# Kernel tuning notes

Hardware: AMD Instinct MI355X
Metric: run time of the kernel (lower is better)

Reference implementation:

```python
import jax, jax.numpy as jnp
import numpy as np

NUM_BINS = 24


def setup_inputs() -> dict:
    key = jax.random.key(0)
    k1, k2 = jax.random.split(key)
    x = jax.random.normal(k1, (64, 1, 512, 512), dtype=jnp.float32)
    y = jax.random.normal(k2, (64, 1, 512, 512), dtype=jnp.float32)
    return {"x": x, "y": y}


def reference(x, y):
    nb = NUM_BINS
    B = x.shape[0]
    # torch.no_grad() downsample -> stop_gradient
    xs = jax.lax.stop_gradient(x[:, :, ::2, ::2])
    ys = jax.lax.stop_gradient(y[:, :, ::2, ::2])
    # small additive noise (randn_like * 1e-4), fixed key for determinism
    nk1, nk2 = jax.random.split(jax.random.key(42))
    xs = xs + jax.random.normal(nk1, xs.shape, xs.dtype) * 0.0001
    ys = ys + jax.random.normal(nk2, ys.shape, ys.dtype) * 0.0001
    x_flat = xs.reshape(B, -1)
    y_flat = ys.reshape(B, -1)
    x_flat = jnp.clip((x_flat + 1.0) * 0.5, 0.001, 0.999)
    y_flat = jnp.clip((y_flat + 1.0) * 0.5, 0.001, 0.999)
    # bucketize against linspace(0,1,nb+1) minus 1 == floor(v*nb), clamped
    x_bin = jnp.clip(jnp.floor(x_flat * nb).astype(jnp.int32), 0, nb - 1)
    y_bin = jnp.clip(jnp.floor(y_flat * nb).astype(jnp.int32), 0, nb - 1)
    # joint histogram for all batches at once via one segment_sum
    batch_off = (jnp.arange(B, dtype=jnp.int32) * (nb * nb))[:, None]
    seg = (batch_off + x_bin * nb + y_bin).reshape(-1)
    ones = jnp.ones(seg.shape, dtype=jnp.float32)
    hist = jax.ops.segment_sum(ones, seg, num_segments=B * nb * nb)
    joint = hist.reshape(B, nb, nb)
    total = joint.sum(axis=(1, 2), keepdims=True) + 1e-10
    joint = joint / total  # [B, nb, nb]
    x_hist = joint.sum(axis=2)  # [B, nb]
    y_hist = joint.sum(axis=1)  # [B, nb]
    eps = 1e-05
    joint_e = joint + eps
    xh = x_hist + eps
    yh = y_hist + eps
    log_joint = jnp.log(joint_e)
    log_prod = jnp.log(xh[:, :, None] * yh[:, None, :])
    mi = jnp.sum(joint_e * (log_joint - log_prod), axis=(1, 2))  # [B]
    hx = -jnp.sum(xh * jnp.log(xh), axis=1)
    hy = -jnp.sum(yh * jnp.log(yh), axis=1)
    se = hx + hy
    nmi = jnp.where(se < 1e-10, 0.0, 2.0 * mi / se)
    nmi = jnp.clip(nmi, -1.0, 1.0)
    return -jnp.clip(jnp.mean(nmi), -1.0, 1.0)
```

## Files before the change

### kernel.cpp

```cpp
#include <hip/hip_runtime.h>
#include <stdint.h>
#include <stddef.h>


#define NB 24
#define NBINS 576
#define NBATCH 64
#define SPB 65536
#define HIST_BPB 16
#define HIST_THREADS 512
#define PER_BLOCK 4096
#define QCAP 1024
#define MARGIN 0.008f

__host__ __device__ __forceinline__ uint32_t rotl32_(uint32_t x, uint32_t r) {
  return (x << r) | (x >> (32u - r));
}

__host__ __device__ inline void threefry2x32_(uint32_t k0, uint32_t k1,
                                              uint32_t& x0, uint32_t& x1) {
  const uint32_t k2 = k0 ^ k1 ^ 0x1BD11BDAu;
  x0 += k0; x1 += k1;
#define TFR(r) { x0 += x1; x1 = rotl32_(x1, (r)); x1 ^= x0; }
  TFR(13u) TFR(15u) TFR(26u) TFR(6u)
  x0 += k1; x1 += k2 + 1u;
  TFR(17u) TFR(29u) TFR(16u) TFR(24u)
  x0 += k2; x1 += k0 + 2u;
  TFR(13u) TFR(15u) TFR(26u) TFR(6u)
  x0 += k0; x1 += k1 + 3u;
  TFR(17u) TFR(29u) TFR(16u) TFR(24u)
  x0 += k1; x1 += k2 + 4u;
  TFR(13u) TFR(15u) TFR(26u) TFR(6u)
  x0 += k2; x1 += k0 + 5u;
#undef TFR
}

__device__ __forceinline__ float erfinv32_(float x) {
  float w = -log1pf(-x * x);
  float p;
  if (w < 5.0f) {
    w -= 2.5f;
    p =  2.81022636e-08f;
    p = fmaf(p, w,  3.43273939e-07f);
    p = fmaf(p, w, -3.5233877e-06f);
    p = fmaf(p, w, -4.39150654e-06f);
    p = fmaf(p, w,  0.00021858087f);
    p = fmaf(p, w, -0.00125372503f);
    p = fmaf(p, w, -0.00417768164f);
    p = fmaf(p, w,  0.246640727f);
    p = fmaf(p, w,  1.50140941f);
  } else {
    w = sqrtf(w) - 3.0f;
    p = -0.000200214257f;
    p = fmaf(p, w,  0.000100950558f);
    p = fmaf(p, w,  0.00134934322f);
    p = fmaf(p, w, -0.00367342844f);
    p = fmaf(p, w,  0.00573950773f);
    p = fmaf(p, w, -0.0076224613f);
    p = fmaf(p, w,  0.00943887047f);
    p = fmaf(p, w,  1.00167406f);
    p = fmaf(p, w,  2.83297682f);
  }
  return p * x;
}

__device__ __forceinline__ float tf_normal_(uint32_t ka, uint32_t kb, uint32_t n) {
  uint32_t x0 = 0u, x1 = n;
  threefry2x32_(ka, kb, x0, x1);
  const uint32_t bits = x0 ^ x1;
  float f = __uint_as_float((bits >> 9) | 0x3F800000u) - 1.0f;
  const float lo = -0.99999994f;
  float u = f * 2.0f + lo;
  u = fmaxf(lo, u);
  return 1.41421356f * erfinv32_(u);
}

__global__ __launch_bounds__(HIST_THREADS) void nmi_hist_kernel(
    const float* __restrict__ x, const float* __restrict__ y,
    uint32_t* __restrict__ ghist,
    uint32_t nk1a, uint32_t nk1b, uint32_t nk2a, uint32_t nk2b) {
  __shared__ uint32_t h[NBINS];
  __shared__ uint16_t q[QCAP];
  __shared__ uint32_t qn;
  for (int t = threadIdx.x; t < NBINS; t += HIST_THREADS) h[t] = 0u;
  if (threadIdx.x == 0) qn = 0u;
  __syncthreads();

  const int b    = blockIdx.x / HIST_BPB;
  const int blk  = blockIdx.x % HIST_BPB;
  const int base = blk * PER_BLOCK;
  const float* __restrict__ xb = x + (size_t)b * 262144;
  const float* __restrict__ yb = y + (size_t)b * 262144;
  const uint32_t nbase = (uint32_t)b * (uint32_t)SPB;

  #pragma unroll
  for (int k = 0; k < PER_BLOCK / HIST_THREADS; ++k) {
    const int i = k * HIST_THREADS + (int)threadIdx.x;
    const int s = base + i;
    const int src = ((s >> 8) << 10) + ((s & 255) << 1);
    const float xv = xb[src];
    const float yv = yb[src];
    const float tx = fminf(fmaxf((xv + 1.0f) * 0.5f, 0.001f), 0.999f) * 24.0f;
    const float ty = fminf(fmaxf((yv + 1.0f) * 0.5f, 0.001f), 0.999f) * 24.0f;
    const float fx = floorf(tx), fy = floorf(ty);
    const float rx = tx - fx,   ry = ty - fy;
    const bool safe = (rx >= MARGIN) & (rx <= 1.0f - MARGIN) &
                      (ry >= MARGIN) & (ry <= 1.0f - MARGIN);
    if (safe) {
      atomicAdd(&h[(int)fx * NB + (int)fy], 1u);
    } else {
      const uint32_t qi = atomicAdd(&qn, 1u);
      if (qi < QCAP) {
        q[qi] = (uint16_t)i;
      } else {
        const uint32_t n = nbase + (uint32_t)s;
        const float xn = xv + tf_normal_(nk1a, nk1b, n) * 1e-4f;
        const float yn = yv + tf_normal_(nk2a, nk2b, n) * 1e-4f;
        const float vx = fminf(fmaxf((xn + 1.0f) * 0.5f, 0.001f), 0.999f);
        const float vy = fminf(fmaxf((yn + 1.0f) * 0.5f, 0.001f), 0.999f);
        int bx = (int)floorf(vx * 24.0f);
        int by = (int)floorf(vy * 24.0f);
        bx = bx < 0 ? 0 : (bx > 23 ? 23 : bx);
        by = by < 0 ? 0 : (by > 23 ? 23 : by);
        atomicAdd(&h[bx * NB + by], 1u);
      }
    }
  }
  __syncthreads();

  const uint32_t nq = qn < QCAP ? qn : (uint32_t)QCAP;
  for (uint32_t j = threadIdx.x; j < nq; j += HIST_THREADS) {
    const int i = (int)q[j];
    const int s = base + i;
    const int src = ((s >> 8) << 10) + ((s & 255) << 1);
    const uint32_t n = nbase + (uint32_t)s;
    const float xn = xb[src] + tf_normal_(nk1a, nk1b, n) * 1e-4f;
    const float yn = yb[src] + tf_normal_(nk2a, nk2b, n) * 1e-4f;
    const float vx = fminf(fmaxf((xn + 1.0f) * 0.5f, 0.001f), 0.999f);
    const float vy = fminf(fmaxf((yn + 1.0f) * 0.5f, 0.001f), 0.999f);
    int bx = (int)floorf(vx * 24.0f);
    int by = (int)floorf(vy * 24.0f);
    bx = bx < 0 ? 0 : (bx > 23 ? 23 : bx);
    by = by < 0 ? 0 : (by > 23 ? 23 : by);
    atomicAdd(&h[bx * NB + by], 1u);
  }
  __syncthreads();

  uint32_t* gh = ghist + b * NBINS;
  for (int t = threadIdx.x; t < NBINS; t += HIST_THREADS) {
    const uint32_t c = h[t];
    if (c) atomicAdd(&gh[t], c);
  }
}

__global__ __launch_bounds__(256) void nmi_reduce_kernel(
    const uint32_t* __restrict__ ghist, float* __restrict__ nmi_arr,
    uint32_t* __restrict__ ctr, float* __restrict__ out) {
  const int b = blockIdx.x;
  __shared__ float joint[NBINS];
  __shared__ float xh[NB];
  __shared__ float yh[NB];
  __shared__ float red_mi[4];
  __shared__ float red_h[4];
  __shared__ int islast;

  const uint32_t* gh = ghist + b * NBINS;
  for (int t = threadIdx.x; t < NBINS; t += 256)
    joint[t] = (float)gh[t] * (1.0f / 65536.0f);
  __syncthreads();

  if (threadIdx.x < NB) {
    const int i = threadIdx.x;
    float sx = 0.f, sy = 0.f;
    for (int j = 0; j < NB; ++j) {
      sx += joint[i * NB + j];
      sy += joint[j * NB + i];
    }
    xh[i] = sx; yh[i] = sy;
  }
  __syncthreads();

  float mi_part = 0.f;
  for (int t = threadIdx.x; t < NBINS; t += 256) {
    const int i = t / NB, j = t % NB;
    const float je = joint[t] + 1e-5f;
    const float pe = (xh[i] + 1e-5f) * (yh[j] + 1e-5f);
    mi_part += je * (logf(je) - logf(pe));
  }
  float h_part = 0.f;
  if (threadIdx.x < NB) {
    const float e = xh[threadIdx.x] + 1e-5f;
    h_part = -(e * logf(e));
  } else if (threadIdx.x >= 64 && threadIdx.x < 64 + NB) {
    const float e = yh[threadIdx.x - 64] + 1e-5f;
    h_part = -(e * logf(e));
  }

  for (int o = 32; o > 0; o >>= 1) {
    mi_part += __shfl_down(mi_part, o);
    h_part  += __shfl_down(h_part, o);
  }
  const int wid  = threadIdx.x >> 6;
  const int lane = threadIdx.x & 63;
  if (lane == 0) { red_mi[wid] = mi_part; red_h[wid] = h_part; }
  __syncthreads();

  if (threadIdx.x == 0) {
    const float mi = red_mi[0] + red_mi[1] + red_mi[2] + red_mi[3];
    const float se = red_h[0] + red_h[1] + red_h[2] + red_h[3];
    float nmi = (se < 1e-10f) ? 0.0f : (2.0f * mi / se);
    nmi = fminf(fmaxf(nmi, -1.0f), 1.0f);
    __hip_atomic_store(&nmi_arr[b], nmi, __ATOMIC_RELEASE,
                       __HIP_MEMORY_SCOPE_AGENT);
    const uint32_t t = __hip_atomic_fetch_add(ctr, 1u, __ATOMIC_ACQ_REL,
                                              __HIP_MEMORY_SCOPE_AGENT);
    islast = (t == (uint32_t)(NBATCH - 1));
  }
  __syncthreads();

  if (islast && threadIdx.x < 64) {
    float v = __hip_atomic_load(&nmi_arr[threadIdx.x], __ATOMIC_ACQUIRE,
                                __HIP_MEMORY_SCOPE_AGENT);
    for (int o = 32; o > 0; o >>= 1) v += __shfl_down(v, o);
    if (threadIdx.x == 0) {
      float m = v * (1.0f / 64.0f);
      m = fminf(fmaxf(m, -1.0f), 1.0f);
      out[0] = -m;
    }
  }
}

extern "C" void kernel_launch(void* const* d_in, const int* in_sizes, int n_in,
                              void* d_out, int out_size, void* d_ws, size_t ws_size,
                              hipStream_t stream) {
  const float* x = (const float*)d_in[0];
  const float* y = (const float*)d_in[1];
  float* out = (float*)d_out;

  uint32_t* ghist = (uint32_t*)d_ws;
  uint32_t* ctr   = (uint32_t*)((char*)d_ws + 147456);
  float*    nmi   = (float*)((char*)d_ws + 147520);

  uint32_t nk1a = 0u, nk1b = 0u; threefry2x32_(0u, 42u, nk1a, nk1b);
  uint32_t nk2a = 0u, nk2b = 1u; threefry2x32_(0u, 42u, nk2a, nk2b);

  hipMemsetAsync(d_ws, 0, 147520 + NBATCH * sizeof(float), stream);
  nmi_hist_kernel<<<NBATCH * HIST_BPB, HIST_THREADS, 0, stream>>>(
      x, y, ghist, nk1a, nk1b, nk2a, nk2b);
  nmi_reduce_kernel<<<NBATCH, 256, 0, stream>>>(ghist, nmi, ctr, out);
}
```

Measured before the change: 138.2 us.

## Fuse histogram and NMI reduction via per-batch last-block completion counters

Merges the histogram and reduce kernels into one launch. Each block writes its partial histogram to its own slot, and the last block per batch (found through an atomic counter) sums the 16 partials and computes the NMI. A global counter lets the final block produce the mean, and the memset shrinks to just the counters. Loads are widened to float4 so each thread handles two strided samples from one vector read, which fetches both even and odd columns and doubles the bytes read per useful sample. The change removes a launch and the global histogram atomics, at the cost of a serialized tail in the last blocks.

```diff
diff --git a/kernel.cpp b/kernel.cpp
--- a/kernel.cpp
+++ b/kernel.cpp
@@ -12,6 +12,11 @@
 #define PER_BLOCK 4096
 #define QCAP 1024
 #define MARGIN 0.008f
+
+#define PART_ELEMS (NBATCH * HIST_BPB * NBINS)
+#define CTR_OFF   ((size_t)PART_ELEMS * 4)
+#define GCTR_OFF  (CTR_OFF + 256)
+#define NMI_OFF   (CTR_OFF + 512)
 
 __host__ __device__ __forceinline__ uint32_t rotl32_(uint32_t x, uint32_t r) {
   return (x << r) | (x >> (32u - r));
@@ -75,15 +80,25 @@
   return 1.41421356f * erfinv32_(u);
 }
 
-__global__ __launch_bounds__(HIST_THREADS) void nmi_hist_kernel(
+__global__ __launch_bounds__(HIST_THREADS) void nmi_fused_kernel(
     const float* __restrict__ x, const float* __restrict__ y,
-    uint32_t* __restrict__ ghist,
+    uint32_t* __restrict__ part, uint32_t* __restrict__ ctr,
+    uint32_t* __restrict__ gctr, float* __restrict__ nmi_arr,
+    float* __restrict__ out,
     uint32_t nk1a, uint32_t nk1b, uint32_t nk2a, uint32_t nk2b) {
   __shared__ uint32_t h[NBINS];
   __shared__ uint16_t q[QCAP];
   __shared__ uint32_t qn;
-  for (int t = threadIdx.x; t < NBINS; t += HIST_THREADS) h[t] = 0u;
-  if (threadIdx.x == 0) qn = 0u;
+  __shared__ int islast, glast;
+  __shared__ float joint[NBINS];
+  __shared__ float xh[NB];
+  __shared__ float yh[NB];
+  __shared__ float red_mi[8];
+  __shared__ float red_h[8];
+
+  const int tid = threadIdx.x;
+  for (int t = tid; t < NBINS; t += HIST_THREADS) h[t] = 0u;
+  if (tid == 0) qn = 0u;
   __syncthreads();
 
   const int b    = blockIdx.x / HIST_BPB;
@@ -94,42 +109,50 @@
   const uint32_t nbase = (uint32_t)b * (uint32_t)SPB;
 
   #pragma unroll
-  for (int k = 0; k < PER_BLOCK / HIST_THREADS; ++k) {
-    const int i = k * HIST_THREADS + (int)threadIdx.x;
-    const int s = base + i;
-    const int src = ((s >> 8) << 10) + ((s & 255) << 1);
-    const float xv = xb[src];
-    const float yv = yb[src];
-    const float tx = fminf(fmaxf((xv + 1.0f) * 0.5f, 0.001f), 0.999f) * 24.0f;
-    const float ty = fminf(fmaxf((yv + 1.0f) * 0.5f, 0.001f), 0.999f) * 24.0f;
-    const float fx = floorf(tx), fy = floorf(ty);
-    const float rx = tx - fx,   ry = ty - fy;
-    const bool safe = (rx >= MARGIN) & (rx <= 1.0f - MARGIN) &
-                      (ry >= MARGIN) & (ry <= 1.0f - MARGIN);
-    if (safe) {
-      atomicAdd(&h[(int)fx * NB + (int)fy], 1u);
-    } else {
-      const uint32_t qi = atomicAdd(&qn, 1u);
-      if (qi < QCAP) {
-        q[qi] = (uint16_t)i;
+  for (int k = 0; k < PER_BLOCK / (2 * HIST_THREADS); ++k) {
+    const int p  = k * HIST_THREADS + tid;
+    const int s0 = base + 2 * p;
+    const int hh = s0 >> 8;
+    const int ww = s0 & 255;
+    const int src = (hh << 10) + (ww << 1);
+    const float4 xv4 = *reinterpret_cast<const float4*>(xb + src);
+    const float4 yv4 = *reinterpret_cast<const float4*>(yb + src);
+    #pragma unroll
+    for (int e = 0; e < 2; ++e) {
+      const float xv = e ? xv4.z : xv4.x;
+      const float yv = e ? yv4.z : yv4.x;
+      const int   i  = 2 * p + e;
+      const float tx = fminf(fmaxf((xv + 1.0f) * 0.5f, 0.001f), 0.999f) * 24.0f;
+      const float ty = fminf(fmaxf((yv + 1.0f) * 0.5f, 0.001f), 0.999f) * 24.0f;
+      const float fx = floorf(tx), fy = floorf(ty);
+      const float rx = tx - fx,   ry = ty - fy;
+      const bool safe = (rx >= MARGIN) & (rx <= 1.0f - MARGIN) &
+                        (ry >= MARGIN) & (ry <= 1.0f - MARGIN);
+      if (safe) {
+        atomicAdd(&h[(int)fx * NB + (int)fy], 1u);
       } else {
-        const uint32_t n = nbase + (uint32_t)s;
-        const float xn = xv + tf_normal_(nk1a, nk1b, n) * 1e-4f;
-        const float yn = yv + tf_normal_(nk2a, nk2b, n) * 1e-4f;
-        const float vx = fminf(fmaxf((xn + 1.0f) * 0.5f, 0.001f), 0.999f);
-        const float vy = fminf(fmaxf((yn + 1.0f) * 0.5f, 0.001f), 0.999f);
-        int bx = (int)floorf(vx * 24.0f);
-        int by = (int)floorf(vy * 24.0f);
-        bx = bx < 0 ? 0 : (bx > 23 ? 23 : bx);
-        by = by < 0 ? 0 : (by > 23 ? 23 : by);
-        atomicAdd(&h[bx * NB + by], 1u);
+        const uint32_t qi = atomicAdd(&qn, 1u);
+        if (qi < QCAP) {
+          q[qi] = (uint16_t)i;
+        } else {
+          const uint32_t n = nbase + (uint32_t)(base + i);
+          const float xn = xv + tf_normal_(nk1a, nk1b, n) * 1e-4f;
+          const float yn = yv + tf_normal_(nk2a, nk2b, n) * 1e-4f;
+          const float vx = fminf(fmaxf((xn + 1.0f) * 0.5f, 0.001f), 0.999f);
+          const float vy = fminf(fmaxf((yn + 1.0f) * 0.5f, 0.001f), 0.999f);
+          int bx = (int)floorf(vx * 24.0f);
+          int by = (int)floorf(vy * 24.0f);
+          bx = bx < 0 ? 0 : (bx > 23 ? 23 : bx);
+          by = by < 0 ? 0 : (by > 23 ? 23 : by);
+          atomicAdd(&h[bx * NB + by], 1u);
+        }
       }
     }
   }
   __syncthreads();
 
   const uint32_t nq = qn < QCAP ? qn : (uint32_t)QCAP;
-  for (uint32_t j = threadIdx.x; j < nq; j += HIST_THREADS) {
+  for (uint32_t j = tid; j < nq; j += HIST_THREADS) {
     const int i = (int)q[j];
     const int s = base + i;
     const int src = ((s >> 8) << 10) + ((s & 255) << 1);
@@ -146,53 +169,54 @@
   }
   __syncthreads();
 
-  uint32_t* gh = ghist + b * NBINS;
-  for (int t = threadIdx.x; t < NBINS; t += HIST_THREADS) {
-    const uint32_t c = h[t];
-    if (c) atomicAdd(&gh[t], c);
-  }
-}
-
-__global__ __launch_bounds__(256) void nmi_reduce_kernel(
-    const uint32_t* __restrict__ ghist, float* __restrict__ nmi_arr,
-    uint32_t* __restrict__ ctr, float* __restrict__ out) {
-  const int b = blockIdx.x;
-  __shared__ float joint[NBINS];
-  __shared__ float xh[NB];
-  __shared__ float yh[NB];
-  __shared__ float red_mi[4];
-  __shared__ float red_h[4];
-  __shared__ int islast;
-
-  const uint32_t* gh = ghist + b * NBINS;
-  for (int t = threadIdx.x; t < NBINS; t += 256)
-    joint[t] = (float)gh[t] * (1.0f / 65536.0f);
-  __syncthreads();
-
-  if (threadIdx.x < NB) {
-    const int i = threadIdx.x;
+  uint32_t* gp = part + (size_t)(b * HIST_BPB + blk) * NBINS;
+  for (int t = tid; t < NBINS; t += HIST_THREADS)
+    __hip_atomic_store(&gp[t], h[t], __ATOMIC_RELAXED,
+                       __HIP_MEMORY_SCOPE_AGENT);
+  __syncthreads();
+
+  if (tid == 0) {
+    const uint32_t t = __hip_atomic_fetch_add(&ctr[b], 1u, __ATOMIC_ACQ_REL,
+                                              __HIP_MEMORY_SCOPE_AGENT);
+    islast = (t == (uint32_t)(HIST_BPB - 1));
+  }
+  __syncthreads();
+  if (!islast) return;
+
+  const uint32_t* pb = part + (size_t)b * HIST_BPB * NBINS;
+  for (int t = tid; t < NBINS; t += HIST_THREADS) {
+    uint32_t c = 0;
+    #pragma unroll
+    for (int sb = 0; sb < HIST_BPB; ++sb)
+      c += __hip_atomic_load(&pb[sb * NBINS + t], __ATOMIC_RELAXED,
+                             __HIP_MEMORY_SCOPE_AGENT);
+    joint[t] = (float)c * (1.0f / 65536.0f);
+  }
+  __syncthreads();
+
+  if (tid < NB) {
     float sx = 0.f, sy = 0.f;
     for (int j = 0; j < NB; ++j) {
-      sx += joint[i * NB + j];
-      sy += joint[j * NB + i];
+      sx += joint[tid * NB + j];
+      sy += joint[j * NB + tid];
     }
-    xh[i] = sx; yh[i] = sy;
+    xh[tid] = sx; yh[tid] = sy;
   }
   __syncthreads();
 
   float mi_part = 0.f;
-  for (int t = threadIdx.x; t < NBINS; t += 256) {
+  for (int t = tid; t < NBINS; t += HIST_THREADS) {
     const int i = t / NB, j = t % NB;
     const float je = joint[t] + 1e-5f;
     const float pe = (xh[i] + 1e-5f) * (yh[j] + 1e-5f);
     mi_part += je * (logf(je) - logf(pe));
   }
   float h_part = 0.f;
-  if (threadIdx.x < NB) {
-    const float e = xh[threadIdx.x] + 1e-5f;
+  if (tid < NB) {
+    const float e = xh[tid] + 1e-5f;
     h_part = -(e * logf(e));
-  } else if (threadIdx.x >= 64 && threadIdx.x < 64 + NB) {
-    const float e = yh[threadIdx.x - 64] + 1e-5f;
+  } else if (tid >= 64 && tid < 64 + NB) {
+    const float e = yh[tid - 64] + 1e-5f;
     h_part = -(e * logf(e));
   }
 
@@ -200,29 +224,30 @@
     mi_part += __shfl_down(mi_part, o);
     h_part  += __shfl_down(h_part, o);
   }
-  const int wid  = threadIdx.x >> 6;
-  const int lane = threadIdx.x & 63;
+  const int wid  = tid >> 6;
+  const int lane = tid & 63;
   if (lane == 0) { red_mi[wid] = mi_part; red_h[wid] = h_part; }
   __syncthreads();
 
-  if (threadIdx.x == 0) {
-    const float mi = red_mi[0] + red_mi[1] + red_mi[2] + red_mi[3];
-    const float se = red_h[0] + red_h[1] + red_h[2] + red_h[3];
+  if (tid == 0) {
+    float mi = 0.f, se = 0.f;
+    #pragma unroll
+    for (int w = 0; w < HIST_THREADS / 64; ++w) { mi += red_mi[w]; se += red_h[w]; }
     float nmi = (se < 1e-10f) ? 0.0f : (2.0f * mi / se);
     nmi = fminf(fmaxf(nmi, -1.0f), 1.0f);
     __hip_atomic_store(&nmi_arr[b], nmi, __ATOMIC_RELEASE,
                        __HIP_MEMORY_SCOPE_AGENT);
-    const uint32_t t = __hip_atomic_fetch_add(ctr, 1u, __ATOMIC_ACQ_REL,
-                                              __HIP_MEMORY_SCOPE_AGENT);
-    islast = (t == (uint32_t)(NBATCH - 1));
-  }
-  __syncthreads();
-
-  if (islast && threadIdx.x < 64) {
-    float v = __hip_atomic_load(&nmi_arr[threadIdx.x], __ATOMIC_ACQUIRE,
+    const uint32_t t2 = __hip_atomic_fetch_add(gctr, 1u, __ATOMIC_ACQ_REL,
+                                               __HIP_MEMORY_SCOPE_AGENT);
+    glast = (t2 == (uint32_t)(NBATCH - 1));
+  }
+  __syncthreads();
+
+  if (glast && tid < 64) {
+    float v = __hip_atomic_load(&nmi_arr[tid], __ATOMIC_ACQUIRE,
                                 __HIP_MEMORY_SCOPE_AGENT);
     for (int o = 32; o > 0; o >>= 1) v += __shfl_down(v, o);
-    if (threadIdx.x == 0) {
+    if (tid == 0) {
       float m = v * (1.0f / 64.0f);
       m = fminf(fmaxf(m, -1.0f), 1.0f);
       out[0] = -m;
@@ -237,15 +262,15 @@
   const float* y = (const float*)d_in[1];
   float* out = (float*)d_out;
 
-  uint32_t* ghist = (uint32_t*)d_ws;
-  uint32_t* ctr   = (uint32_t*)((char*)d_ws + 147456);
-  float*    nmi   = (float*)((char*)d_ws + 147520);
+  uint32_t* part = (uint32_t*)d_ws;
+  uint32_t* ctr  = (uint32_t*)((char*)d_ws + CTR_OFF);
+  uint32_t* gctr = (uint32_t*)((char*)d_ws + GCTR_OFF);
+  float*    nmi  = (float*)((char*)d_ws + NMI_OFF);
 
   uint32_t nk1a = 0u, nk1b = 0u; threefry2x32_(0u, 42u, nk1a, nk1b);
   uint32_t nk2a = 0u, nk2b = 1u; threefry2x32_(0u, 42u, nk2a, nk2b);
 
-  hipMemsetAsync(d_ws, 0, 147520 + NBATCH * sizeof(float), stream);
-  nmi_hist_kernel<<<NBATCH * HIST_BPB, HIST_THREADS, 0, stream>>>(
-      x, y, ghist, nk1a, nk1b, nk2a, nk2b);
-  nmi_reduce_kernel<<<NBATCH, 256, 0, stream>>>(ghist, nmi, ctr, out);
-}
+  hipMemsetAsync((char*)d_ws + CTR_OFF, 0, 260, stream);
+  nmi_fused_kernel<<<NBATCH * HIST_BPB, HIST_THREADS, 0, stream>>>(
+      x, y, part, ctr, gctr, nmi, out, nk1a, nk1b, nk2a, nk2b);
+}
```

Measured after the change: 186.0 us. 34.6% more time.
